# Performance work log

Hardware: AMD Instinct MI355X
Metric: run time of the kernel (lower is better)

## Reference

```python
import math
import jax, jax.numpy as jnp
import numpy as np

D = 192      # d_model
NH = 8       # heads
NL = 2       # levels
NP = 4       # points
HD = D // NH # head dim = 24
GROUPS = 32


def layer_norm(x, g, b, eps=1e-5):
    mu = x.mean(-1, keepdims=True)
    var = ((x - mu) ** 2).mean(-1, keepdims=True)
    return (x - mu) / jnp.sqrt(var + eps) * g + b


def group_norm(x, g, b, eps=1e-5):
    # x: [B, C, H, W]
    B, C, H, W = x.shape
    xg = x.reshape(B, GROUPS, C // GROUPS, H, W)
    mu = xg.mean((2, 3, 4), keepdims=True)
    var = ((xg - mu) ** 2).mean((2, 3, 4), keepdims=True)
    xn = ((xg - mu) / jnp.sqrt(var + eps)).reshape(B, C, H, W)
    return xn * g[None, :, None, None] + b[None, :, None, None]


def pos_embed_2d(H, W):
    # PositionalEncoding2D(96, normalize=True) with an all-valid mask
    eps = 1e-6
    scale = 2 * math.pi
    npf = 96
    y = (jnp.arange(1, H + 1, dtype=jnp.float32) - 0.5) / (H + eps) * scale
    x = (jnp.arange(1, W + 1, dtype=jnp.float32) - 0.5) / (W + eps) * scale
    dim_t = 10000.0 ** (2.0 * (jnp.arange(npf) // 2).astype(jnp.float32) / npf)
    def enc(v):
        p = v[:, None] / dim_t  # [N, 96]
        return jnp.stack([jnp.sin(p[:, 0::2]), jnp.cos(p[:, 1::2])], -1).reshape(v.shape[0], npf)
    pe_y, pe_x = enc(y), enc(x)
    pos = jnp.concatenate([
        jnp.broadcast_to(pe_y[:, None, :], (H, W, npf)),
        jnp.broadcast_to(pe_x[None, :, :], (H, W, npf)),
    ], -1)  # [H, W, 192] (y-part first, like torch cat((pos_y, pos_x)))
    return pos.reshape(H * W, 2 * npf)


def ms_sample(value_h, loc, H, W):
    # value_h: [B, NH, H*W, HD]; loc: [B, NH, Lq, NP, 2] normalized to [0,1]
    # Replicates F.grid_sample(mode='bilinear', padding_mode='zeros', align_corners=False)
    B, _, Lq, P, _ = loc.shape
    x = loc[..., 0] * W - 0.5
    y = loc[..., 1] * H - 0.5
    x0 = jnp.floor(x)
    y0 = jnp.floor(y)
    wx = x - x0
    wy = y - y0
    def corner(xc, yc, w):
        valid = (xc >= 0) & (xc <= W - 1) & (yc >= 0) & (yc <= H - 1)
        xi = jnp.clip(xc, 0, W - 1).astype(jnp.int32)
        yi = jnp.clip(yc, 0, H - 1).astype(jnp.int32)
        idx = (yi * W + xi).reshape(B, NH, Lq * P)
        g = jnp.take_along_axis(value_h, idx[..., None], axis=2).reshape(B, NH, Lq, P, HD)
        return g * (w * valid)[..., None]
    return (corner(x0, y0, (1 - wx) * (1 - wy))
            + corner(x0 + 1, y0, wx * (1 - wy))
            + corner(x0, y0 + 1, (1 - wx) * wy)
            + corner(x0 + 1, y0 + 1, wx * wy))


def encoder_forward(src, pos, ref_pts, shapes, p):
    B, L, _ = src.shape
    starts = np.cumsum([0] + [h * w for h, w in shapes])
    offset_norm = jnp.array([[w, h] for h, w in shapes], jnp.float32)  # [NL, 2] = (W, H)
    out = src
    n_layers = p['so_W'].shape[0]
    for i in range(n_layers):
        q = out + pos
        off = (q @ p['so_W'][i] + p['so_b'][i]).reshape(B, L, NH, NL, NP, 2)
        aw = (q @ p['aw_W'][i] + p['aw_b'][i]).reshape(B, L, NH, NL * NP)
        aw = jax.nn.softmax(aw, -1).reshape(B, L, NH, NL, NP)
        loc = ref_pts[None, :, None, :, None, :] + off / offset_norm[None, None, None, :, None, :]
        v = (out @ p['vp_W'][i] + p['vp_b'][i]).reshape(B, L, NH, HD).transpose(0, 2, 1, 3)
        sampled = []
        for l, (h, w) in enumerate(shapes):
            vl = v[:, :, starts[l]:starts[l + 1], :]
            locl = loc[:, :, :, l].transpose(0, 2, 1, 3, 4)  # [B, NH, L, NP, 2]
            sampled.append(ms_sample(vl, locl, h, w))
        sampled = jnp.stack(sampled, 3)  # [B, NH, L, NL, NP, HD]
        awh = aw.transpose(0, 2, 1, 3, 4)  # [B, NH, L, NL, NP]
        attn = jnp.einsum('bhqlp,bhqlpc->bhqc', awh, sampled)
        attn = attn.transpose(0, 2, 1, 3).reshape(B, L, D)
        attn = attn @ p['op_W'][i] + p['op_b'][i]
        out = layer_norm(out + attn, p['ln1_g'][i], p['ln1_b'][i])
        ff = jax.nn.relu(out @ p['l1_W'][i] + p['l1_b'][i]) @ p['l2_W'][i] + p['l2_b'][i]
        out = layer_norm(out + ff, p['ln2_g'][i], p['ln2_b'][i])
    return out


def _feature_encoder(feat0, feat1, proj_w0, proj_b0, gn_g0, gn_b0,
                     proj_w1, proj_b1, gn_g1, gn_b1, level_embed, p):
    feats = [feat0, feat1]
    projs = [(proj_w0, proj_b0, gn_g0, gn_b0), (proj_w1, proj_b1, gn_g1, gn_b1)]
    shapes = [(int(f.shape[2]), int(f.shape[3])) for f in feats]
    B = feat0.shape[0]
    srcs, poss, refs = [], [], []
    for l, f in enumerate(feats):
        w, b, g, bb = projs[l]
        s = jnp.einsum('bchw,oc->bohw', f, w) + b[None, :, None, None]  # 1x1 conv
        s = group_norm(s, g, bb)
        srcs.append(s.reshape(B, D, -1).transpose(0, 2, 1))
        poss.append(pos_embed_2d(*shapes[l]) + level_embed[l])
        h, wdt = shapes[l]
        ry, rx = jnp.meshgrid(jnp.linspace(0.5, h - 0.5, h) / h,
                              jnp.linspace(0.5, wdt - 0.5, wdt) / wdt, indexing='ij')
        refs.append(jnp.stack([rx.reshape(-1), ry.reshape(-1)], -1))
    src = jnp.concatenate(srcs, 1)                # [B, Ltot, D]
    pos = jnp.concatenate(poss, 0)[None]          # [1, Ltot, D]
    # full-size images => masks all False => valid_ratios == 1
    ref_pts = jnp.broadcast_to(jnp.concatenate(refs, 0)[:, None, :], (src.shape[1], NL, 2))
    mem = encoder_forward(src, pos, ref_pts, shapes, p)
    n0 = shapes[0][0] * shapes[0][1]
    m0 = mem[:, :n0].reshape(B, shapes[0][0], shapes[0][1], D).transpose(0, 3, 1, 2)
    m1 = mem[:, n0:].reshape(B, shapes[1][0], shapes[1][1], D).transpose(0, 3, 1, 2)
    return m0, m1


def setup_inputs() -> dict:
    key = jax.random.key(0)
    ks = jax.random.split(key, 20)
    L = 6
    s = 0.02
    d = {}
    d['feat0'] = jax.random.normal(ks[0], (2, D, 96, 96), jnp.float32)
    d['feat1'] = jax.random.normal(ks[1], (2, D, 48, 48), jnp.float32)
    d['imgs'] = jax.random.normal(ks[2], (2, 3, 384, 384), jnp.float32)
    d['proj_w0'] = jax.random.normal(ks[3], (D, D), jnp.float32) * s
    d['proj_b0'] = jnp.zeros((D,), jnp.float32)
    d['gn_g0'] = jnp.ones((D,), jnp.float32)
    d['gn_b0'] = jnp.zeros((D,), jnp.float32)
    d['proj_w1'] = jax.random.normal(ks[4], (D, D), jnp.float32) * s
    d['proj_b1'] = jnp.zeros((D,), jnp.float32)
    d['gn_g1'] = jnp.ones((D,), jnp.float32)
    d['gn_b1'] = jnp.zeros((D,), jnp.float32)
    d['level_embed'] = jax.random.normal(ks[5], (NL, D), jnp.float32) * s
    d['so_W'] = jax.random.normal(ks[6], (L, D, NH * NL * NP * 2), jnp.float32) * s
    d['so_b'] = jax.random.normal(ks[7], (L, NH * NL * NP * 2), jnp.float32) * s
    d['aw_W'] = jax.random.normal(ks[8], (L, D, NH * NL * NP), jnp.float32) * s
    d['aw_b'] = jnp.zeros((L, NH * NL * NP), jnp.float32)
    d['vp_W'] = jax.random.normal(ks[9], (L, D, D), jnp.float32) * s
    d['vp_b'] = jnp.zeros((L, D), jnp.float32)
    d['op_W'] = jax.random.normal(ks[10], (L, D, D), jnp.float32) * s
    d['op_b'] = jnp.zeros((L, D), jnp.float32)
    d['ln1_g'] = jnp.ones((L, D), jnp.float32)
    d['ln1_b'] = jnp.zeros((L, D), jnp.float32)
    d['l1_W'] = jax.random.normal(ks[11], (L, D, 256), jnp.float32) * s
    d['l1_b'] = jnp.zeros((L, 256), jnp.float32)
    d['l2_W'] = jax.random.normal(ks[12], (L, 256, D), jnp.float32) * s
    d['l2_b'] = jnp.zeros((L, D), jnp.float32)
    d['ln2_g'] = jnp.ones((L, D), jnp.float32)
    d['ln2_b'] = jnp.zeros((L, D), jnp.float32)
    return d


def reference(feat0, feat1, imgs, proj_w0, proj_b0, gn_g0, gn_b0,
              proj_w1, proj_b1, gn_g1, gn_b1, level_embed,
              so_W, so_b, aw_W, aw_b, vp_W, vp_b, op_W, op_b,
              ln1_g, ln1_b, l1_W, l1_b, l2_W, l2_b, ln2_g, ln2_b):
    # imgs is only used for image sizes; full-size => all-valid masks
    p = dict(so_W=so_W, so_b=so_b, aw_W=aw_W, aw_b=aw_b, vp_W=vp_W, vp_b=vp_b,
             op_W=op_W, op_b=op_b, ln1_g=ln1_g, ln1_b=ln1_b,
             l1_W=l1_W, l1_b=l1_b, l2_W=l2_W, l2_b=l2_b, ln2_g=ln2_g, ln2_b=ln2_b)
    return _feature_encoder(feat0, feat1, proj_w0, proj_b0, gn_g0, gn_b0,
                            proj_w1, proj_b1, gn_g1, gn_b1, level_embed, p)
```

## Files before the change

kernel.cpp:

```cpp
#include <hip/hip_runtime.h>
#include <hip/hip_bf16.h>
#include <math.h>

#define Bb 2
#define Dm 192
#define NHh 8
#define HDd 24
#define N0 9216
#define N1 2304
#define LSEQ 11520
#define FFD 256
#define Mrows (Bb*LSEQ)

typedef __attribute__((ext_vector_type(8))) short short8;
typedef __attribute__((ext_vector_type(4))) float f32x4;

#define F_OUT 0
#define F_PRE (F_OUT + 4423680)
#define F_POS (F_PRE + 4423680)
#define F_LOC (F_POS + 2211840)
#define F_AW  (F_LOC + 2949120)
#define F_QB  (F_AW + 1474560)
#define F_OB  (F_QB + 2211840)
#define F_AH  (F_OB + 2211840)
#define F_WT16 (F_AH + 2949120)
#define F_BC  (F_WT16 + 626688)
#define F_GNS (F_BC + 1152)

#define WL_STRIDE 208896
#define WL_SOAW 0
#define WL_VP   36864
#define WL_OP   73728
#define WL_L1   110592
#define WL_L2   159744

__device__ inline __hip_bfloat16 f2b(float f) { return __float2bfloat16(f); }
__device__ inline unsigned short f2bu(float f) {
    __hip_bfloat16 h = __float2bfloat16(f);
    return *reinterpret_cast<unsigned short*>(&h);
}
__device__ inline float u2f(unsigned short u) {
    unsigned int x = ((unsigned int)u) << 16;
    return __uint_as_float(x);
}

__global__ void k_pos(float* pos, const float* level_embed) {
    int idx = blockIdx.x * 256 + threadIdx.x;
    if (idx >= LSEQ * Dm) return;
    int t = idx / Dm, d = idx % Dm;
    int lvl, row, col, H, W;
    if (t < N0) { lvl = 0; H = 96; W = 96; row = t / 96; col = t % 96; }
    else        { lvl = 1; H = 48; W = 48; int tl = t - N0; row = tl / 48; col = tl % 48; }
    int k = d % 96;
    float v;
    if (d < 96) v = (row + 0.5f) / ((float)H + 1e-6f) * 6.2831853071795864f;
    else        v = (col + 0.5f) / ((float)W + 1e-6f) * 6.2831853071795864f;
    float expo = (float)(k - (k & 1)) / 96.0f;
    float tm = exp2f(expo * 13.287712379549449f);
    float p = v / tm;
    float pe = (k & 1) ? cosf(p) : sinf(p);
    pos[idx] = pe + level_embed[lvl * Dm + d];
}

__global__ void k_prep(const float* soW, const float* awW, const float* vpW,
        const float* opW, const float* l1W, const float* l2W,
        const float* sob, const float* awb,
        __hip_bfloat16* WT, float* BC) {
    int idx = blockIdx.x * 256 + threadIdx.x;
    if (idx < 6 * 192) {
        int i = idx / 192, n = idx % 192;
        BC[idx] = (n < 128) ? sob[i * 128 + n] : awb[i * 64 + (n - 128)];
    }
    if (idx >= 6 * WL_STRIDE) return;
    int i = idx / WL_STRIDE; int r = idx % WL_STRIDE;
    float v;
    if (r < 36864)       { int n = r / 192, k = r % 192;
        v = (n < 128) ? soW[((size_t)i * 192 + k) * 128 + n]
                      : awW[((size_t)i * 192 + k) * 64 + (n - 128)]; }
    else if (r < 73728)  { int q = r - 36864;  int n = q / 192, k = q % 192;
        v = vpW[((size_t)i * 192 + k) * 192 + n]; }
    else if (r < 110592) { int q = r - 73728;  int n = q / 192, k = q % 192;
        v = opW[((size_t)i * 192 + k) * 192 + n]; }
    else if (r < 159744) { int q = r - 110592; int n = q / 192, k = q % 192;
        v = l1W[((size_t)i * 192 + k) * 256 + n]; }
    else                 { int q = r - 159744; int n = q / 256, k = q % 256;
        v = l2W[((size_t)i * 256 + k) * 192 + n]; }
    WT[idx] = f2b(v);
}

__global__ void k_prepc(const float* w0, const float* w1, __hip_bfloat16* cwb) {
    int idx = blockIdx.x * 256 + threadIdx.x;
    if (idx >= 2 * 36864) return;
    const float* w = (idx < 36864) ? w0 : w1;
    int r = idx % 36864;
    cwb[idx] = f2b(w[r]);
}

__global__ void k_tf(const float* feat, __hip_bfloat16* out, int HW, int st) {
    __shared__ float tile[32][33];
    int t0 = blockIdx.x * 32, c0 = blockIdx.y * 32, b = blockIdx.z;
    int tx = threadIdx.x, ty = threadIdx.y;
    #pragma unroll
    for (int k = 0; k < 4; k++) {
        int c = c0 + ty + k * 8;
        tile[ty + k * 8][tx] = feat[((size_t)b * Dm + c) * HW + t0 + tx];
    }
    __syncthreads();
    #pragma unroll
    for (int k = 0; k < 4; k++) {
        int t = t0 + ty + k * 8;
        out[((size_t)b * LSEQ + st + t) * Dm + c0 + tx] = f2b(tile[tx][ty + k * 8]);
    }
}

__global__ __launch_bounds__(192) void k_gnp(const float* __restrict__ pre,
        float* __restrict__ part) {
    int bid = blockIdx.x;
    int b = bid / 120; int r = bid % 120;
    int l = (r >= 96) ? 1 : 0; int ch = l ? (r - 96) : r;
    int start = b * LSEQ + (l ? N0 : 0) + ch * 96;
    int d = threadIdx.x;
    float s = 0.f, sq = 0.f;
    for (int t = 0; t < 96; t++) {
        float x = pre[(size_t)(start + t) * Dm + d];
        s += x; sq += x * x;
    }
    __shared__ float ls[192], lq[192];
    ls[d] = s; lq[d] = sq;
    __syncthreads();
    if (d < 32) {
        float a = 0.f, b2 = 0.f;
        #pragma unroll
        for (int j = 0; j < 6; j++) { a += ls[d * 6 + j]; b2 += lq[d * 6 + j]; }
        part[((size_t)bid * 32 + d) * 2]     = a;
        part[((size_t)bid * 32 + d) * 2 + 1] = b2;
    }
}

__global__ void k_gnf(const float* __restrict__ part, float* __restrict__ gns) {
    int bid = blockIdx.x;
    int b = bid >> 6; int l = (bid >> 5) & 1; int g = bid & 31;
    int nch = l ? 24 : 96;
    int base = b * 120 + (l ? 96 : 0);
    int tid = threadIdx.x;
    float s = 0.f, q = 0.f;
    for (int c = tid; c < nch; c += 64) {
        s += part[((size_t)(base + c) * 32 + g) * 2];
        q += part[((size_t)(base + c) * 32 + g) * 2 + 1];
    }
    for (int m = 1; m < 64; m <<= 1) { s += __shfl_xor(s, m, 64); q += __shfl_xor(q, m, 64); }
    if (tid == 0) {
        float total = (float)((l ? N1 : N0) * 6);
        float mean = s / total;
        float var = q / total - mean * mean;
        gns[bid * 2] = mean;
        gns[bid * 2 + 1] = rsqrtf(var + 1e-5f);
    }
}

__global__ void k_gnnorm(const float* srcp, const float* gns,
        const float* g0, const float* b0, const float* g1, const float* b1,
        const float* pos, float* out, __hip_bfloat16* ob, __hip_bfloat16* qb) {
    int idx = blockIdx.x * 256 + threadIdx.x;
    if (idx >= Bb * LSEQ * Dm) return;
    int d = idx % Dm;
    int t = (idx / Dm) % LSEQ;
    int l = (t < N0) ? 0 : 1;
    int g = d / 6;
    int b = idx / (Dm * LSEQ);
    int sid = ((b * 2 + l) * 32 + g) * 2;
    float mean = gns[sid], rstd = gns[sid + 1];
    float gg = l ? g1[d] : g0[d];
    float bbv = l ? b1[d] : b0[d];
    float v = (srcp[idx] - mean) * rstd * gg + bbv;
    out[idx] = v;
    ob[idx] = f2b(v);
    qb[idx] = f2b(v + pos[idx - (size_t)b * LSEQ * Dm]);
}

template<int KSTEPS>
__global__ __launch_bounds__(256) void k_gemm(
        const __hip_bfloat16* __restrict__ A,
        const __hip_bfloat16* __restrict__ Bt,
        const float* __restrict__ bias,
        float* __restrict__ Cf, int N) {
    constexpr int K = KSTEPS * 32;
    int wid = threadIdx.x >> 6, lane = threadIdx.x & 63;
    int lg = lane >> 4, lr = lane & 15;
    int row0 = blockIdx.x * 64 + wid * 16;
    int col0 = blockIdx.y * 64;
    const short* a_base = (const short*)A + (size_t)(row0 + lr) * K + lg * 8;
    const short* b_base = (const short*)Bt + (size_t)(col0 + lr) * K + lg * 8;
    f32x4 acc[4] = {};
    #pragma unroll
    for (int kk = 0; kk < KSTEPS; kk++) {
        short8 af = *(const short8*)(a_base + kk * 32);
        #pragma unroll
        for (int n = 0; n < 4; n++) {
            short8 bfr = *(const short8*)(b_base + (size_t)n * 16 * K + kk * 32);
            acc[n] = __builtin_amdgcn_mfma_f32_16x16x32_bf16(af, bfr, acc[n], 0, 0, 0);
        }
    }
    #pragma unroll
    for (int n = 0; n < 4; n++) {
        int col = col0 + n * 16 + lr;
        float bv = bias[col];
        #pragma unroll
        for (int r = 0; r < 4; r++) {
            int row = row0 + lg * 4 + r;
            Cf[(size_t)row * N + col] = acc[n][r] + bv;
        }
    }
}

__global__ __launch_bounds__(192) void k_soawvp(
        const __hip_bfloat16* __restrict__ QB,
        const __hip_bfloat16* __restrict__ OB,
        const __hip_bfloat16* __restrict__ BtS,
        const __hip_bfloat16* __restrict__ BtV,
        const float* __restrict__ biasS,
        const float* __restrict__ biasV,
        float* __restrict__ LOC, float* __restrict__ AW,
        __hip_bfloat16* __restrict__ VB) {
    constexpr int K = 192;
    int wid = threadIdx.x >> 6, lane = threadIdx.x & 63;
    int lg = lane >> 4, lr = lane & 15;
    int row0 = blockIdx.x * 16;
    int col0 = wid * 64;
    int role = blockIdx.y;
    const short* A  = (const short*)(role ? OB : QB);
    const short* Bt = (const short*)(role ? BtV : BtS);
    const float* bias = role ? biasV : biasS;
    const short* a_base = A + (size_t)(row0 + lr) * K + lg * 8;
    const short* b_base = Bt + (size_t)(col0 + lr) * K + lg * 8;
    f32x4 acc[4] = {};
    #pragma unroll
    for (int kk = 0; kk < 6; kk++) {
        short8 af = *(const short8*)(a_base + kk * 32);
        #pragma unroll
        for (int n = 0; n < 4; n++) {
            short8 bfr = *(const short8*)(b_base + (size_t)n * 16 * K + kk * 32);
            acc[n] = __builtin_amdgcn_mfma_f32_16x16x32_bf16(af, bfr, acc[n], 0, 0, 0);
        }
    }
    #pragma unroll
    for (int n = 0; n < 4; n++) {
        float bv = bias[col0 + n * 16 + lr];
        #pragma unroll
        for (int r = 0; r < 4; r++) acc[n][r] += bv;
    }
    if (role) {
        #pragma unroll
        for (int n = 0; n < 4; n++) {
            int col = col0 + n * 16 + lr;
            #pragma unroll
            for (int r = 0; r < 4; r++)
                VB[(size_t)(row0 + lg * 4 + r) * Dm + col] = f2b(acc[n][r]);
        }
    } else if (wid == 2) {
        #pragma unroll
        for (int n = 0; n < 4; n++) {
            #pragma unroll
            for (int r = 0; r < 4; r++) {
                float v = acc[n][r];
                float m = v;
                m = fmaxf(m, __shfl_xor(m, 1)); m = fmaxf(m, __shfl_xor(m, 2));
                m = fmaxf(m, __shfl_xor(m, 4));
                float e = expf(v - m);
                float sm = e;
                sm += __shfl_xor(sm, 1); sm += __shfl_xor(sm, 2); sm += __shfl_xor(sm, 4);
                AW[(size_t)(row0 + lg * 4 + r) * 64 + n * 16 + lr] = e / sm;
            }
        }
    } else {
        #pragma unroll
        for (int r = 0; r < 4; r++) {
            int row = row0 + lg * 4 + r;
            int t = (row >= LSEQ) ? row - LSEQ : row;
            int rr, cc, Ht, Wt;
            if (t < N0) { Ht = 96; Wt = 96; rr = t / 96; cc = t % 96; }
            else        { Ht = 48; Wt = 48; int tl = t - N0; rr = tl / 48; cc = tl % 48; }
            float refx = (cc + 0.5f) / (float)Wt;
            float refy = (rr + 0.5f) / (float)Ht;
            #pragma unroll
            for (int n = 0; n < 4; n++) {
                int col = col0 + n * 16 + lr;
                int j = col >> 1, comp = col & 1;
                float sc = (j & 4) ? 48.f : 96.f;
                LOC[(size_t)row * 128 + col] = (comp ? refy : refx) + acc[n][r] / sc;
            }
        }
    }
}

__global__ __launch_bounds__(256) void k_tail(
        const __hip_bfloat16* __restrict__ ATT,
        const __hip_bfloat16* __restrict__ BtOp, const float* __restrict__ bOp,
        const __hip_bfloat16* __restrict__ Bt1, const float* __restrict__ b1,
        const __hip_bfloat16* __restrict__ Bt2, const float* __restrict__ b2,
        const float* __restrict__ g1, const float* __restrict__ t1,
        const float* __restrict__ g2, const float* __restrict__ t2,
        const float* __restrict__ pos,
        float* __restrict__ OUTp, __hip_bfloat16* __restrict__ ob,
        __hip_bfloat16* __restrict__ qb) {
    __shared__ __align__(16) short ybf[16][200];
    __shared__ __align__(16) short hid[16][264];
    __shared__ float y32[16][196];
    __shared__ float ps[4][16], pq[4][16];
    int tid = threadIdx.x;
    int wid = tid >> 6, lane = tid & 63, lg = lane >> 4, lr = lane & 15;
    int row0 = blockIdx.x * 16;
    {
        const short* a_base = (const short*)ATT + (size_t)(row0 + lr) * 192 + lg * 8;
        const short* b_base = (const short*)BtOp + (size_t)(wid * 48 + lr) * 192 + lg * 8;
        f32x4 acc[3] = {};
        #pragma unroll
        for (int kk = 0; kk < 6; kk++) {
            short8 af = *(const short8*)(a_base + kk * 32);
            #pragma unroll
            for (int n = 0; n < 3; n++) {
                short8 bfr = *(const short8*)(b_base + (size_t)n * 16 * 192 + kk * 32);
                acc[n] = __builtin_amdgcn_mfma_f32_16x16x32_bf16(af, bfr, acc[n], 0, 0, 0);
            }
        }
        float s[4] = {0.f, 0.f, 0.f, 0.f}, q[4] = {0.f, 0.f, 0.f, 0.f};
        #pragma unroll
        for (int n = 0; n < 3; n++) {
            int col = wid * 48 + n * 16 + lr;
            float bv = bOp[col];
            #pragma unroll
            for (int r = 0; r < 4; r++) {
                size_t o = (size_t)(row0 + lg * 4 + r) * Dm + col;
                float v = acc[n][r] + bv + OUTp[o];
                acc[n][r] = v;
                s[r] += v; q[r] += v * v;
            }
        }
        #pragma unroll
        for (int r = 0; r < 4; r++) {
            #pragma unroll
            for (int m = 1; m < 16; m <<= 1) {
                s[r] += __shfl_xor(s[r], m); q[r] += __shfl_xor(q[r], m);
            }
        }
        if (lr == 0) {
            #pragma unroll
            for (int r = 0; r < 4; r++) { ps[wid][lg * 4 + r] = s[r]; pq[wid][lg * 4 + r] = q[r]; }
        }
        __syncthreads();
        float mean[4], rstd[4];
        #pragma unroll
        for (int r = 0; r < 4; r++) {
            int r16 = lg * 4 + r;
            float S = ps[0][r16] + ps[1][r16] + ps[2][r16] + ps[3][r16];
            float Q = pq[0][r16] + pq[1][r16] + pq[2][r16] + pq[3][r16];
            mean[r] = S * (1.f / Dm);
            float var = Q * (1.f / Dm) - mean[r] * mean[r];
            rstd[r] = rsqrtf(var + 1e-5f);
        }
        #pragma unroll
        for (int n = 0; n < 3; n++) {
            int col = wid * 48 + n * 16 + lr;
            float gg = g1[col], bb = t1[col];
            #pragma unroll
            for (int r = 0; r < 4; r++) {
                int rl = lg * 4 + r;
                float y = (acc[n][r] - mean[r]) * rstd[r] * gg + bb;
                y32[rl][col] = y;
                ybf[rl][col] = (short)f2bu(y);
            }
        }
        __syncthreads();
    }
    {
        const short* b_base = (const short*)Bt1 + (size_t)(wid * 64 + lr) * 192 + lg * 8;
        f32x4 acc[4] = {};
        #pragma unroll
        for (int kk = 0; kk < 6; kk++) {
            short8 af = *(const short8*)&ybf[lr][lg * 8 + kk * 32];
            #pragma unroll
            for (int n = 0; n < 4; n++) {
                short8 bfr = *(const short8*)(b_base + (size_t)n * 16 * 192 + kk * 32);
                acc[n] = __builtin_amdgcn_mfma_f32_16x16x32_bf16(af, bfr, acc[n], 0, 0, 0);
            }
        }
        #pragma unroll
        for (int n = 0; n < 4; n++) {
            int col = wid * 64 + n * 16 + lr;
            float bv = b1[col];
            #pragma unroll
            for (int r = 0; r < 4; r++)
                hid[lg * 4 + r][col] = (short)f2bu(fmaxf(acc[n][r] + bv, 0.f));
        }
        __syncthreads();
    }
    {
        const short* b_base = (const short*)Bt2 + (size_t)(wid * 48 + lr) * 256 + lg * 8;
        f32x4 acc[3] = {};
        #pragma unroll
        for (int kk = 0; kk < 8; kk++) {
            short8 af = *(const short8*)&hid[lr][lg * 8 + kk * 32];
            #pragma unroll
            for (int n = 0; n < 3; n++) {
                short8 bfr = *(const short8*)(b_base + (size_t)n * 16 * 256 + kk * 32);
                acc[n] = __builtin_amdgcn_mfma_f32_16x16x32_bf16(af, bfr, acc[n], 0, 0, 0);
            }
        }
        float s[4] = {0.f, 0.f, 0.f, 0.f}, q[4] = {0.f, 0.f, 0.f, 0.f};
        #pragma unroll
        for (int n = 0; n < 3; n++) {
            int col = wid * 48 + n * 16 + lr;
            float bv = b2[col];
            #pragma unroll
            for (int r = 0; r < 4; r++) {
                float v = acc[n][r] + bv + y32[lg * 4 + r][col];
                acc[n][r] = v;
                s[r] += v; q[r] += v * v;
            }
        }
        #pragma unroll
        for (int r = 0; r < 4; r++) {
            #pragma unroll
            for (int m = 1; m < 16; m <<= 1) {
                s[r] += __shfl_xor(s[r], m); q[r] += __shfl_xor(q[r], m);
            }
        }
        if (lr == 0) {
            #pragma unroll
            for (int r = 0; r < 4; r++) { ps[wid][lg * 4 + r] = s[r]; pq[wid][lg * 4 + r] = q[r]; }
        }
        __syncthreads();
        float mean[4], rstd[4];
        #pragma unroll
        for (int r = 0; r < 4; r++) {
            int r16 = lg * 4 + r;
            float S = ps[0][r16] + ps[1][r16] + ps[2][r16] + ps[3][r16];
            float Q = pq[0][r16] + pq[1][r16] + pq[2][r16] + pq[3][r16];
            mean[r] = S * (1.f / Dm);
            float var = Q * (1.f / Dm) - mean[r] * mean[r];
            rstd[r] = rsqrtf(var + 1e-5f);
        }
        #pragma unroll
        for (int n = 0; n < 3; n++) {
            int col = wid * 48 + n * 16 + lr;
            float gg = g2[col], bb = t2[col];
            #pragma unroll
            for (int r = 0; r < 4; r++) {
                int row = row0 + lg * 4 + r;
                size_t o = (size_t)row * Dm + col;
                float y = (acc[n][r] - mean[r]) * rstd[r] * gg + bb;
                OUTp[o] = y;
                ob[o] = f2b(y);
                int tp = (row >= LSEQ) ? row - LSEQ : row;
                qb[o] = f2b(y + pos[(size_t)tp * Dm + col]);
            }
        }
    }
}

__global__ __launch_bounds__(192) void k_sample(const __hip_bfloat16* __restrict__ V,
        const float* __restrict__ LOC, const float* __restrict__ AW,
        __hip_bfloat16* __restrict__ ATT) {
    __shared__ float aw_s[4][64];
    __shared__ float loc_s[4][128];
    int tid = threadIdx.x;
    int tg0 = blockIdx.x * 4;
    for (int idx = tid; idx < 256; idx += 192)
        aw_s[idx >> 6][idx & 63] = AW[(size_t)tg0 * 64 + idx];
    for (int idx = tid; idx < 512; idx += 192)
        loc_s[idx >> 7][idx & 127] = LOC[(size_t)tg0 * 128 + idx];
    __syncthreads();
    int tt = tid / 48, lane = tid - tt * 48;
    int h = lane / 6, dq = lane - h * 6;
    int tg = tg0 + tt;
    int b = (tg >= LSEQ) ? 1 : 0;
    const unsigned short* vb = (const unsigned short*)V + (size_t)b * LSEQ * Dm + h * HDd + dq * 4;
    float a0 = 0.f, a1 = 0.f, a2 = 0.f, a3 = 0.f;
    #pragma unroll
    for (int lp = 0; lp < 8; lp++) {
        int l = lp >> 2;
        int Wl = l ? 48 : 96, Hl = l ? 48 : 96, st = l ? N0 : 0;
        float a  = aw_s[tt][h * 8 + lp];
        float lx = loc_s[tt][(h * 8 + lp) * 2];
        float ly = loc_s[tt][(h * 8 + lp) * 2 + 1];
        float x = lx * (float)Wl - 0.5f, y = ly * (float)Hl - 0.5f;
        float x0f = floorf(x), y0f = floorf(y);
        float wx = x - x0f, wy = y - y0f;
        int x0 = (int)x0f, y0 = (int)y0f;
        #pragma unroll
        for (int cy = 0; cy < 2; cy++) {
            int yi = y0 + cy;
            float wyv = cy ? wy : 1.f - wy;
            bool vy = (yi >= 0) && (yi < Hl);
            int yc = min(max(yi, 0), Hl - 1);
            #pragma unroll
            for (int cx = 0; cx < 2; cx++) {
                int xi = x0 + cx;
                float wv = (cx ? wx : 1.f - wx) * wyv;
                bool ok = vy && (xi >= 0) && (xi < Wl);
                int xc = min(max(xi, 0), Wl - 1);
                float cw = ok ? a * wv : 0.f;
                ushort4 g4 = *(const ushort4*)(vb + (size_t)(st + yc * Wl + xc) * Dm);
                a0 += cw * u2f(g4.x); a1 += cw * u2f(g4.y);
                a2 += cw * u2f(g4.z); a3 += cw * u2f(g4.w);
            }
        }
    }
    ushort4 o4;
    o4.x = f2bu(a0); o4.y = f2bu(a1); o4.z = f2bu(a2); o4.w = f2bu(a3);
    *(ushort4*)((unsigned short*)ATT + (size_t)tg * Dm + h * HDd + dq * 4) = o4;
}

__global__ void k_outt(const float* __restrict__ out, float* __restrict__ dst,
        int HW, int st) {
    __shared__ float tile[32][33];
    int t0 = blockIdx.x * 32, d0 = blockIdx.y * 32, b = blockIdx.z;
    int tx = threadIdx.x, ty = threadIdx.y;
    #pragma unroll
    for (int k = 0; k < 4; k++) {
        int t = t0 + ty + k * 8;
        tile[ty + k * 8][tx] = out[((size_t)b * LSEQ + st + t) * Dm + d0 + tx];
    }
    __syncthreads();
    #pragma unroll
    for (int k = 0; k < 4; k++) {
        int d = d0 + ty + k * 8;
        dst[((size_t)b * Dm + d) * HW + t0 + tx] = tile[tx][ty + k * 8];
    }
}

extern "C" void kernel_launch(void* const* d_in, const int* in_sizes, int n_in,
                              void* d_out, int out_size, void* d_ws, size_t ws_size,
                              hipStream_t stream) {
    (void)in_sizes; (void)n_in; (void)out_size; (void)ws_size;
    const float* feat0   = (const float*)d_in[0];
    const float* feat1   = (const float*)d_in[1];
    const float* proj_w0 = (const float*)d_in[3];
    const float* proj_b0 = (const float*)d_in[4];
    const float* gn_g0   = (const float*)d_in[5];
    const float* gn_b0   = (const float*)d_in[6];
    const float* proj_w1 = (const float*)d_in[7];
    const float* proj_b1 = (const float*)d_in[8];
    const float* gn_g1   = (const float*)d_in[9];
    const float* gn_b1   = (const float*)d_in[10];
    const float* level_embed = (const float*)d_in[11];
    const float* so_W = (const float*)d_in[12];
    const float* so_b = (const float*)d_in[13];
    const float* aw_W = (const float*)d_in[14];
    const float* aw_b = (const float*)d_in[15];
    const float* vp_W = (const float*)d_in[16];
    const float* vp_b = (const float*)d_in[17];
    const float* op_W = (const float*)d_in[18];
    const float* op_b = (const float*)d_in[19];
    const float* ln1_g = (const float*)d_in[20];
    const float* ln1_b = (const float*)d_in[21];
    const float* l1_W = (const float*)d_in[22];
    const float* l1_b = (const float*)d_in[23];
    const float* l2_W = (const float*)d_in[24];
    const float* l2_b = (const float*)d_in[25];
    const float* ln2_g = (const float*)d_in[26];
    const float* ln2_b = (const float*)d_in[27];

    float* ws   = (float*)d_ws;
    float* OUT  = ws + F_OUT;
    float* PRE  = ws + F_PRE;
    float* POS  = ws + F_POS;
    float* LOC  = ws + F_LOC;
    float* AWp  = ws + F_AW;
    __hip_bfloat16* QB  = (__hip_bfloat16*)(ws + F_QB);
    __hip_bfloat16* OB  = (__hip_bfloat16*)(ws + F_OB);
    __hip_bfloat16* AH  = (__hip_bfloat16*)(ws + F_AH);
    __hip_bfloat16* WT16 = (__hip_bfloat16*)(ws + F_WT16);
    __hip_bfloat16* VB  = (__hip_bfloat16*)(ws + F_PRE);
    float* BC   = ws + F_BC;
    float* GNS  = ws + F_GNS;
    __hip_bfloat16* FEATB = (__hip_bfloat16*)(ws + F_LOC);
    __hip_bfloat16* CWB   = (__hip_bfloat16*)(ws + F_AW);
    float* GPART = ws + F_AH;

    k_pos<<<(LSEQ * Dm + 255) / 256, 256, 0, stream>>>(POS, level_embed);
    k_prep<<<(6 * WL_STRIDE + 255) / 256, 256, 0, stream>>>(so_W, aw_W, vp_W, op_W,
        l1_W, l2_W, so_b, aw_b, WT16, BC);
    k_prepc<<<(2 * 36864 + 255) / 256, 256, 0, stream>>>(proj_w0, proj_w1, CWB);
    k_tf<<<dim3(N0 / 32, 6, 2), dim3(32, 8), 0, stream>>>(feat0, FEATB, N0, 0);
    k_tf<<<dim3(N1 / 32, 6, 2), dim3(32, 8), 0, stream>>>(feat1, FEATB, N1, N0);
    for (int b = 0; b < 2; b++) {
        k_gemm<6><<<dim3(N0 / 64, 3), 256, 0, stream>>>(
            FEATB + (size_t)b * LSEQ * Dm, CWB, proj_b0,
            PRE + (size_t)b * LSEQ * Dm, Dm);
        k_gemm<6><<<dim3(N1 / 64, 3), 256, 0, stream>>>(
            FEATB + ((size_t)b * LSEQ + N0) * Dm, CWB + 36864, proj_b1,
            PRE + ((size_t)b * LSEQ + N0) * Dm, Dm);
    }
    k_gnp<<<240, 192, 0, stream>>>(PRE, GPART);
    k_gnf<<<128, 64, 0, stream>>>(GPART, GNS);
    k_gnnorm<<<(Bb * LSEQ * Dm + 255) / 256, 256, 0, stream>>>(PRE, GNS,
        gn_g0, gn_b0, gn_g1, gn_b1, POS, OUT, OB, QB);

    for (int i = 0; i < 6; i++) {
        const __hip_bfloat16* WL = WT16 + (size_t)i * WL_STRIDE;
        k_soawvp<<<dim3(Mrows / 16, 2), 192, 0, stream>>>(
            QB, OB, WL + WL_SOAW, WL + WL_VP, BC + i * 192,
            vp_b + (size_t)i * Dm, LOC, AWp, VB);
        k_sample<<<Mrows / 4, 192, 0, stream>>>(VB, LOC, AWp, AH);
        k_tail<<<Mrows / 16, 256, 0, stream>>>(
            AH, WL + WL_OP, op_b + (size_t)i * Dm,
            WL + WL_L1, l1_b + (size_t)i * FFD,
            WL + WL_L2, l2_b + (size_t)i * Dm,
            ln1_g + (size_t)i * Dm, ln1_b + (size_t)i * Dm,
            ln2_g + (size_t)i * Dm, ln2_b + (size_t)i * Dm, POS,
            OUT, OB, QB);
    }
    k_outt<<<dim3(N0 / 32, 6, 2), dim3(32, 8), 0, stream>>>(OUT, (float*)d_out, N0, 0);
    k_outt<<<dim3(N1 / 32, 6, 2), dim3(32, 8), 0, stream>>>(OUT,
        (float*)d_out + (size_t)Bb * Dm * N0, N1, N0);
}
```

Before: 759.7 us.

## Keep value projection in fp32, double rows per soawvp block, prefetch residual

The value projection output is now stored as fp32 in the PRE buffer instead of bf16, so the sampler gathers float4 and skips the bf16 unpacking. The soawvp kernel loads its B-weight fragments into registers once and reuses them across two 16-row groups, halving the grid and cutting weight reloads. The tail kernel loads residual values before the MFMA loop so their latency overlaps compute. The risks are doubled gather bandwidth in the sampler and higher register pressure from holding 24 short8 weight fragments.

New measurement: 745.9 us. Within noise of the previous version (-1.8%).

```diff
diff --git a/kernel.cpp b/kernel.cpp
--- a/kernel.cpp
+++ b/kernel.cpp
@@ -38,10 +38,6 @@
 __device__ inline unsigned short f2bu(float f) {
     __hip_bfloat16 h = __float2bfloat16(f);
     return *reinterpret_cast<unsigned short*>(&h);
-}
-__device__ inline float u2f(unsigned short u) {
-    unsigned int x = ((unsigned int)u) << 16;
-    return __uint_as_float(x);
 }
 
 __global__ void k_pos(float* pos, const float* level_embed) {
@@ -221,73 +217,83 @@
         const float* __restrict__ biasS,
         const float* __restrict__ biasV,
         float* __restrict__ LOC, float* __restrict__ AW,
-        __hip_bfloat16* __restrict__ VB) {
+        float* __restrict__ VF) {
     constexpr int K = 192;
     int wid = threadIdx.x >> 6, lane = threadIdx.x & 63;
     int lg = lane >> 4, lr = lane & 15;
-    int row0 = blockIdx.x * 16;
+    int row0 = blockIdx.x * 32;
     int col0 = wid * 64;
     int role = blockIdx.y;
     const short* A  = (const short*)(role ? OB : QB);
     const short* Bt = (const short*)(role ? BtV : BtS);
     const float* bias = role ? biasV : biasS;
-    const short* a_base = A + (size_t)(row0 + lr) * K + lg * 8;
-    const short* b_base = Bt + (size_t)(col0 + lr) * K + lg * 8;
-    f32x4 acc[4] = {};
-    #pragma unroll
-    for (int kk = 0; kk < 6; kk++) {
-        short8 af = *(const short8*)(a_base + kk * 32);
+    short8 bw[24];
+    {
+        const short* b_base = Bt + (size_t)(col0 + lr) * K + lg * 8;
+        #pragma unroll
+        for (int n = 0; n < 4; n++)
+            #pragma unroll
+            for (int kk = 0; kk < 6; kk++)
+                bw[n * 6 + kk] = *(const short8*)(b_base + (size_t)n * 16 * K + kk * 32);
+    }
+    #pragma unroll
+    for (int rg = 0; rg < 2; rg++) {
+        const short* a_base = A + (size_t)(row0 + rg * 16 + lr) * K + lg * 8;
+        f32x4 acc[4] = {};
+        #pragma unroll
+        for (int kk = 0; kk < 6; kk++) {
+            short8 af = *(const short8*)(a_base + kk * 32);
+            #pragma unroll
+            for (int n = 0; n < 4; n++)
+                acc[n] = __builtin_amdgcn_mfma_f32_16x16x32_bf16(af, bw[n * 6 + kk], acc[n], 0, 0, 0);
+        }
         #pragma unroll
         for (int n = 0; n < 4; n++) {
-            short8 bfr = *(const short8*)(b_base + (size_t)n * 16 * K + kk * 32);
-            acc[n] = __builtin_amdgcn_mfma_f32_16x16x32_bf16(af, bfr, acc[n], 0, 0, 0);
-        }
-    }
-    #pragma unroll
-    for (int n = 0; n < 4; n++) {
-        float bv = bias[col0 + n * 16 + lr];
-        #pragma unroll
-        for (int r = 0; r < 4; r++) acc[n][r] += bv;
-    }
-    if (role) {
-        #pragma unroll
-        for (int n = 0; n < 4; n++) {
-            int col = col0 + n * 16 + lr;
-            #pragma unroll
-            for (int r = 0; r < 4; r++)
-                VB[(size_t)(row0 + lg * 4 + r) * Dm + col] = f2b(acc[n][r]);
-        }
-    } else if (wid == 2) {
-        #pragma unroll
-        for (int n = 0; n < 4; n++) {
-            #pragma unroll
-            for (int r = 0; r < 4; r++) {
-                float v = acc[n][r];
-                float m = v;
-                m = fmaxf(m, __shfl_xor(m, 1)); m = fmaxf(m, __shfl_xor(m, 2));
-                m = fmaxf(m, __shfl_xor(m, 4));
-                float e = expf(v - m);
-                float sm = e;
-                sm += __shfl_xor(sm, 1); sm += __shfl_xor(sm, 2); sm += __shfl_xor(sm, 4);
-                AW[(size_t)(row0 + lg * 4 + r) * 64 + n * 16 + lr] = e / sm;
-            }
-        }
-    } else {
-        #pragma unroll
-        for (int r = 0; r < 4; r++) {
-            int row = row0 + lg * 4 + r;
-            int t = (row >= LSEQ) ? row - LSEQ : row;
-            int rr, cc, Ht, Wt;
-            if (t < N0) { Ht = 96; Wt = 96; rr = t / 96; cc = t % 96; }
-            else        { Ht = 48; Wt = 48; int tl = t - N0; rr = tl / 48; cc = tl % 48; }
-            float refx = (cc + 0.5f) / (float)Wt;
-            float refy = (rr + 0.5f) / (float)Ht;
+            float bv = bias[col0 + n * 16 + lr];
+            #pragma unroll
+            for (int r = 0; r < 4; r++) acc[n][r] += bv;
+        }
+        int rbase = row0 + rg * 16;
+        if (role) {
             #pragma unroll
             for (int n = 0; n < 4; n++) {
                 int col = col0 + n * 16 + lr;
-                int j = col >> 1, comp = col & 1;
-                float sc = (j & 4) ? 48.f : 96.f;
-                LOC[(size_t)row * 128 + col] = (comp ? refy : refx) + acc[n][r] / sc;
+                #pragma unroll
+                for (int r = 0; r < 4; r++)
+                    VF[(size_t)(rbase + lg * 4 + r) * Dm + col] = acc[n][r];
+            }
+        } else if (wid == 2) {
+            #pragma unroll
+            for (int n = 0; n < 4; n++) {
+                #pragma unroll
+                for (int r = 0; r < 4; r++) {
+                    float v = acc[n][r];
+                    float m = v;
+                    m = fmaxf(m, __shfl_xor(m, 1)); m = fmaxf(m, __shfl_xor(m, 2));
+                    m = fmaxf(m, __shfl_xor(m, 4));
+                    float e = expf(v - m);
+                    float sm = e;
+                    sm += __shfl_xor(sm, 1); sm += __shfl_xor(sm, 2); sm += __shfl_xor(sm, 4);
+                    AW[(size_t)(rbase + lg * 4 + r) * 64 + n * 16 + lr] = e / sm;
+                }
+            }
+        } else {
+            #pragma unroll
+            for (int r = 0; r < 4; r++) {
+                int row = rbase + lg * 4 + r;
+                int t = (row >= LSEQ) ? row - LSEQ : row;
+                int rr, cc, Ht, Wt;
+                if (t < N0) { Ht = 96; Wt = 96; rr = t / 96; cc = t % 96; }
+                else        { Ht = 48; Wt = 48; int tl = t - N0; rr = tl / 48; cc = tl % 48; }
+                float refx = (cc + 0.5f) / (float)Wt;
+                float refy = (rr + 0.5f) / (float)Ht;
+                #pragma unroll
+                for (int n = 0; n < 4; n++) {
+                    int col = col0 + n * 16 + lr;
+                    int j = col >> 1, comp = col & 1;
+                    float sc = (j & 4) ? 48.f : 96.f;
+                    LOC[(size_t)row * 128 + col] = (comp ? refy : refx) + acc[n][r] / sc;
+                }
             }
         }
     }
@@ -311,6 +317,14 @@
     int wid = tid >> 6, lane = tid & 63, lg = lane >> 4, lr = lane & 15;
     int row0 = blockIdx.x * 16;
     {
+        float resid[3][4];
+        #pragma unroll
+        for (int n = 0; n < 3; n++) {
+            int col = wid * 48 + n * 16 + lr;
+            #pragma unroll
+            for (int r = 0; r < 4; r++)
+                resid[n][r] = OUTp[(size_t)(row0 + lg * 4 + r) * Dm + col];
+        }
         const short* a_base = (const short*)ATT + (size_t)(row0 + lr) * 192 + lg * 8;
         const short* b_base = (const short*)BtOp + (size_t)(wid * 48 + lr) * 192 + lg * 8;
         f32x4 acc[3] = {};
@@ -330,8 +344,7 @@
             float bv = bOp[col];
             #pragma unroll
             for (int r = 0; r < 4; r++) {
-                size_t o = (size_t)(row0 + lg * 4 + r) * Dm + col;
-                float v = acc[n][r] + bv + OUTp[o];
+                float v = acc[n][r] + bv + resid[n][r];
                 acc[n][r] = v;
                 s[r] += v; q[r] += v * v;
             }
@@ -458,7 +471,7 @@
     }
 }
 
-__global__ __launch_bounds__(192) void k_sample(const __hip_bfloat16* __restrict__ V,
+__global__ __launch_bounds__(192) void k_sample(const float* __restrict__ V,
         const float* __restrict__ LOC, const float* __restrict__ AW,
         __hip_bfloat16* __restrict__ ATT) {
     __shared__ float aw_s[4][64];
@@ -474,7 +487,7 @@
     int h = lane / 6, dq = lane - h * 6;
     int tg = tg0 + tt;
     int b = (tg >= LSEQ) ? 1 : 0;
-    const unsigned short* vb = (const unsigned short*)V + (size_t)b * LSEQ * Dm + h * HDd + dq * 4;
+    const float* vb = V + (size_t)b * LSEQ * Dm + h * HDd + dq * 4;
     float a0 = 0.f, a1 = 0.f, a2 = 0.f, a3 = 0.f;
     #pragma unroll
     for (int lp = 0; lp < 8; lp++) {
@@ -500,9 +513,9 @@
                 bool ok = vy && (xi >= 0) && (xi < Wl);
                 int xc = min(max(xi, 0), Wl - 1);
                 float cw = ok ? a * wv : 0.f;
-                ushort4 g4 = *(const ushort4*)(vb + (size_t)(st + yc * Wl + xc) * Dm);
-                a0 += cw * u2f(g4.x); a1 += cw * u2f(g4.y);
-                a2 += cw * u2f(g4.z); a3 += cw * u2f(g4.w);
+                float4 g4 = *(const float4*)(vb + (size_t)(st + yc * Wl + xc) * Dm);
+                a0 += cw * g4.x; a1 += cw * g4.y;
+                a2 += cw * g4.z; a3 += cw * g4.w;
             }
         }
     }
@@ -571,7 +584,6 @@
     __hip_bfloat16* OB  = (__hip_bfloat16*)(ws + F_OB);
     __hip_bfloat16* AH  = (__hip_bfloat16*)(ws + F_AH);
     __hip_bfloat16* WT16 = (__hip_bfloat16*)(ws + F_WT16);
-    __hip_bfloat16* VB  = (__hip_bfloat16*)(ws + F_PRE);
     float* BC   = ws + F_BC;
     float* GNS  = ws + F_GNS;
     __hip_bfloat16* FEATB = (__hip_bfloat16*)(ws + F_LOC);
@@ -599,10 +611,10 @@
 
     for (int i = 0; i < 6; i++) {
         const __hip_bfloat16* WL = WT16 + (size_t)i * WL_STRIDE;
-        k_soawvp<<<dim3(Mrows / 16, 2), 192, 0, stream>>>(
+        k_soawvp<<<dim3(Mrows / 32, 2), 192, 0, stream>>>(
             QB, OB, WL + WL_SOAW, WL + WL_VP, BC + i * 192,
-            vp_b + (size_t)i * Dm, LOC, AWp, VB);
-        k_sample<<<Mrows / 4, 192, 0, stream>>>(VB, LOC, AWp, AH);
+            vp_b + (size_t)i * Dm, LOC, AWp, PRE);
+        k_sample<<<Mrows / 4, 192, 0, stream>>>(PRE, LOC, AWp, AH);
         k_tail<<<Mrows / 16, 256, 0, stream>>>(
             AH, WL + WL_OP, op_b + (size_t)i * Dm,
             WL + WL_L1, l1_b + (size_t)i * FFD,
```
